# Kernel tuning notes

Hardware: AMD Instinct MI355X
Metric: run time of the kernel (lower is better)

The kernel has to match this reference:

```python
import jax, jax.numpy as jnp
import numpy as np

NUM_NODES = 200000   # graph size
E = 128              # embedding_size
B = 256              # batch of target nodes
M = 8                # num_metapaths
L = 64               # walk length (number of (n1,n2,e) triples per metapath)
NUM_EDGE_TYPE = 8
H = 8                # num_heads (hardcoded in module)


def setup_inputs() -> dict:
    key = jax.random.key(0)
    ks = jax.random.split(key, 10)
    # walks: last dim = (n1, n2, edge_type)
    n12 = jax.random.randint(ks[0], (B, M, L, 2), 0, NUM_NODES)
    ety = jax.random.randint(ks[1], (B, M, L, 1), 0, NUM_EDGE_TYPE)
    node_mp_walks = jnp.concatenate([n12, ety], axis=-1)
    node_idx = jax.random.randint(ks[2], (B,), 0, NUM_NODES)
    mp_type_idx = jnp.arange(M)
    # fc1(onehot(n)) == node_table[n] + fc1_b  (node_table = fc1.weight.T)
    node_table = jax.random.normal(ks[3], (NUM_NODES, E), dtype=jnp.float32) * 0.1
    fc1_b = jnp.zeros((E,), dtype=jnp.float32)
    edge_table = jax.random.normal(ks[4], (NUM_EDGE_TYPE, E), dtype=jnp.float32) * 0.1
    # Indexed_LinearFC_List: one (E,E) linear per metapath
    W_mp = jax.random.normal(ks[5], (M, E, E), dtype=jnp.float32) * 0.05
    b_mp = jnp.zeros((M, E), dtype=jnp.float32)
    # MultiheadAttention params (embed_dim=E, num_heads=H, eval mode -> no dropout)
    Wqkv = jax.random.normal(ks[6], (3 * E, E), dtype=jnp.float32) * 0.05
    bqkv = jnp.zeros((3 * E,), dtype=jnp.float32)
    Wo = jax.random.normal(ks[7], (E, E), dtype=jnp.float32) * 0.05
    bo = jnp.zeros((E,), dtype=jnp.float32)
    return dict(node_idx=node_idx, mp_type_idx=mp_type_idx, node_mp_walks=node_mp_walks,
                node_table=node_table, fc1_b=fc1_b, edge_table=edge_table,
                W_mp=W_mp, b_mp=b_mp, Wqkv=Wqkv, bqkv=bqkv, Wo=Wo, bo=bo)


def reference(node_idx, mp_type_idx, node_mp_walks, node_table, fc1_b, edge_table,
              W_mp, b_mp, Wqkv, bqkv, Wo, bo):
    n1 = node_mp_walks[..., 0]          # [B,M,L]
    n2 = node_mp_walks[..., 1]
    e = node_mp_walks[..., 2]
    # gather node/edge embeddings (fc1 over one-hot == table row + bias)
    n1_vec = node_table[n1] + fc1_b     # [B,M,L,E]
    n2_vec = node_table[n2] + fc1_b     # [B,M,L,E]
    edge_vec = edge_table[e]            # [B,M,L,E]
    # elementwise fuse + mean over walk steps
    mp_agg_0 = jnp.mean(n1_vec * n2_vec * edge_vec, axis=2)        # [B,M,E]
    # per-metapath indexed linear
    Wsel = W_mp[mp_type_idx]            # [M,E,E]
    bsel = b_mp[mp_type_idx]            # [M,E]
    mp_agg_1 = jnp.einsum('bme,meo->bmo', mp_agg_0, Wsel) + bsel   # [B,M,E]
    # self-attention over metapaths (torch MHA, seq-first layout: [M,B,E])
    x = jnp.transpose(mp_agg_1, (1, 0, 2))                         # [M,B,E]
    qkv = x @ Wqkv.T + bqkv                                        # [M,B,3E]
    q, k, v = jnp.split(qkv, 3, axis=-1)
    hd = E // H
    q = q.reshape(M, B, H, hd)
    k = k.reshape(M, B, H, hd)
    v = v.reshape(M, B, H, hd)
    scores = jnp.einsum('mbhd,nbhd->bhmn', q, k) / jnp.sqrt(jnp.float32(hd))
    attn = jax.nn.softmax(scores, axis=-1)                         # [B,H,M,M]
    o = jnp.einsum('bhmn,nbhd->mbhd', attn, v).reshape(M, B, E)
    attn_output = o @ Wo.T + bo                                    # [M,B,E]
    return attn_output
```

## Files before the change

### kernel.cpp

```cpp
#include <hip/hip_runtime.h>

#define B 256
#define M 8
#define L 64
#define E 128
#define H 8
#define HD 16
#define NET 8
#define E3 384

__global__ __launch_bounds__(256) void k_transpose(
    const float* __restrict__ Wqkv, const float* __restrict__ Wo,
    float* __restrict__ WqkvT, float* __restrict__ WoT) {
  int idx = blockIdx.x * 256 + threadIdx.x;
  if (idx < E * E3) {
    int e = idx / E3;
    int o = idx - e * E3;
    WqkvT[idx] = Wqkv[o * E + e];
  } else {
    int j = idx - E * E3;
    int e = j >> 7, o = j & 127;
    WoT[j] = Wo[o * E + e];
  }
}

__global__ __launch_bounds__(256) void k_gather(
    const int* __restrict__ walks, const float* __restrict__ node_table,
    const float* __restrict__ fc1_b, const float* __restrict__ edge_table,
    float* __restrict__ agg0) {
  __shared__ int s_idx[L * 3];
  __shared__ float s_et[NET * E];
  __shared__ float4 s_red[256];

  int r = blockIdx.x;
  int t = threadIdx.x;
  int g = t >> 5, lane = t & 31;

  if (t < L * 3) s_idx[t] = walks[r * (L * 3) + t];
  for (int i = t; i < NET * E; i += 256) s_et[i] = edge_table[i];
  __syncthreads();

  const float4* nt4 = (const float4*)node_table;
  float4 fb = ((const float4*)fc1_b)[lane];
  float4 acc = make_float4(0.f, 0.f, 0.f, 0.f);

  #pragma unroll
  for (int i = 0; i < 8; ++i) {
    int l = (i << 3) + g;
    int n1 = s_idx[3 * l];
    int n2 = s_idx[3 * l + 1];
    int et = s_idx[3 * l + 2];
    float4 a = nt4[n1 * 32 + lane];
    float4 c = nt4[n2 * 32 + lane];
    float4 ev = ((const float4*)(s_et + et * E))[lane];
    acc.x += (a.x + fb.x) * (c.x + fb.x) * ev.x;
    acc.y += (a.y + fb.y) * (c.y + fb.y) * ev.y;
    acc.z += (a.z + fb.z) * (c.z + fb.z) * ev.z;
    acc.w += (a.w + fb.w) * (c.w + fb.w) * ev.w;
  }
  s_red[t] = acc;
  __syncthreads();
  if (t < 32) {
    float4 s = s_red[t];
    #pragma unroll
    for (int gg = 1; gg < 8; ++gg) {
      float4 v = s_red[gg * 32 + t];
      s.x += v.x; s.y += v.y; s.z += v.z; s.w += v.w;
    }
    const float inv = 1.0f / (float)L;
    s.x *= inv; s.y *= inv; s.z *= inv; s.w *= inv;
    ((float4*)agg0)[r * 32 + t] = s;
  }
}

__global__ __launch_bounds__(128) void k_mplinear(
    const float* __restrict__ agg0, const int* __restrict__ mp_type_idx,
    const float* __restrict__ W_mp, const float* __restrict__ b_mp,
    float* __restrict__ agg1) {
  __shared__ float xs[8][E];
  int t = threadIdx.x;
  int m = blockIdx.y;
  int b0 = blockIdx.x * 8;
  int mp = mp_type_idx[m];
  #pragma unroll
  for (int j = 0; j < 8; ++j)
    xs[j][t] = agg0[((b0 + j) * M + m) * E + t];
  __syncthreads();
  float acc[8] = {0, 0, 0, 0, 0, 0, 0, 0};
  const float* W = W_mp + mp * E * E;
  for (int e = 0; e < E; ++e) {
    float w = W[e * E + t];
    #pragma unroll
    for (int j = 0; j < 8; ++j) acc[j] += xs[j][e] * w;
  }
  float bias = b_mp[mp * E + t];
  #pragma unroll
  for (int j = 0; j < 8; ++j)
    agg1[((b0 + j) * M + m) * E + t] = acc[j] + bias;
}

__global__ __launch_bounds__(128) void k_qkv(
    const float* __restrict__ agg1, const float* __restrict__ WqkvT,
    const float* __restrict__ bqkv, float* __restrict__ qkv) {
  __shared__ float xs[8][E];
  int t = threadIdx.x;
  int r0 = blockIdx.x * 8;
  int o = blockIdx.y * E + t;
  #pragma unroll
  for (int j = 0; j < 8; ++j)
    xs[j][t] = agg1[(r0 + j) * E + t];
  __syncthreads();
  float acc[8] = {0, 0, 0, 0, 0, 0, 0, 0};
  for (int e = 0; e < E; ++e) {
    float w = WqkvT[e * E3 + o];
    #pragma unroll
    for (int j = 0; j < 8; ++j) acc[j] += xs[j][e] * w;
  }
  float bias = bqkv[o];
  #pragma unroll
  for (int j = 0; j < 8; ++j)
    qkv[(r0 + j) * E3 + o] = acc[j] + bias;
}

__global__ __launch_bounds__(256) void k_attn(
    const float* __restrict__ qkv, const float* __restrict__ WoT,
    const float* __restrict__ bo, float* __restrict__ out) {
  __shared__ float s_qkv[M][E3 + 1];
  __shared__ float s_sc[H][M][M];
  __shared__ float s_o[M][E];
  int b = blockIdx.x;
  int t = threadIdx.x;

  #pragma unroll
  for (int i = 0; i < 12; ++i) {
    int idx = i * 256 + t;
    int mt = idx / E3;
    int col = idx - mt * E3;
    s_qkv[mt][col] = qkv[(b * M + mt) * E3 + col];
  }
  __syncthreads();

  #pragma unroll
  for (int i = 0; i < 2; ++i) {
    int idx = i * 256 + t;
    int h = idx >> 6;
    int mq = (idx >> 3) & 7;
    int n = idx & 7;
    float s = 0.f;
    #pragma unroll
    for (int d = 0; d < HD; ++d)
      s += s_qkv[mq][h * HD + d] * s_qkv[n][E + h * HD + d];
    s_sc[h][mq][n] = s * 0.25f;
  }
  __syncthreads();

  if (t < 64) {
    int h = t >> 3, mq = t & 7;
    float mx = -1e30f;
    #pragma unroll
    for (int n = 0; n < 8; ++n) mx = fmaxf(mx, s_sc[h][mq][n]);
    float ex[8];
    float sum = 0.f;
    #pragma unroll
    for (int n = 0; n < 8; ++n) { ex[n] = __expf(s_sc[h][mq][n] - mx); sum += ex[n]; }
    float inv = 1.0f / sum;
    #pragma unroll
    for (int n = 0; n < 8; ++n) s_sc[h][mq][n] = ex[n] * inv;
  }
  __syncthreads();

  #pragma unroll
  for (int i = 0; i < 4; ++i) {
    int idx = i * 256 + t;
    int mq = idx >> 7;
    int col = idx & 127;
    int h = col >> 4;
    float s = 0.f;
    #pragma unroll
    for (int n = 0; n < 8; ++n)
      s += s_sc[h][mq][n] * s_qkv[n][2 * E + col];
    s_o[mq][col] = s;
  }
  __syncthreads();

  int o = t & 127;
  int mbase = t >> 7;
  float accp[4] = {0, 0, 0, 0};
  for (int e = 0; e < E; ++e) {
    float w = WoT[e * E + o];
    #pragma unroll
    for (int i = 0; i < 4; ++i)
      accp[i] += s_o[2 * i + mbase][e] * w;
  }
  float bias = bo[o];
  #pragma unroll
  for (int i = 0; i < 4; ++i) {
    int mq = 2 * i + mbase;
    out[(mq * B + b) * E + o] = accp[i] + bias;
  }
}

extern "C" void kernel_launch(void* const* d_in, const int* in_sizes, int n_in,
                              void* d_out, int out_size, void* d_ws, size_t ws_size,
                              hipStream_t stream) {
  const int*   mp_type_idx = (const int*)d_in[1];
  const int*   walks       = (const int*)d_in[2];
  const float* node_table  = (const float*)d_in[3];
  const float* fc1_b       = (const float*)d_in[4];
  const float* edge_table  = (const float*)d_in[5];
  const float* W_mp        = (const float*)d_in[6];
  const float* b_mp        = (const float*)d_in[7];
  const float* Wqkv        = (const float*)d_in[8];
  const float* bqkv        = (const float*)d_in[9];
  const float* Wo          = (const float*)d_in[10];
  const float* bo          = (const float*)d_in[11];
  float* out = (float*)d_out;

  char* ws = (char*)d_ws;
  float* agg0  = (float*)(ws);
  float* agg1  = (float*)(ws + (1 << 20));
  float* qkvb  = (float*)(ws + (2 << 20));
  float* WqkvT = (float*)(ws + (5 << 20));
  float* WoT   = (float*)(ws + (5 << 20) + (256 << 10));

  k_transpose<<<dim3(256), dim3(256), 0, stream>>>(Wqkv, Wo, WqkvT, WoT);
  k_gather<<<dim3(B * M), dim3(256), 0, stream>>>(walks, node_table, fc1_b, edge_table, agg0);
  k_mplinear<<<dim3(32, 8), dim3(128), 0, stream>>>(agg0, mp_type_idx, W_mp, b_mp, agg1);
  k_qkv<<<dim3(256, 3), dim3(128), 0, stream>>>(agg1, WqkvT, bqkv, qkvb);
  k_attn<<<dim3(B), dim3(256), 0, stream>>>(qkvb, WoT, bo, out);
}
```

Measured before the change: 211.2 us.

## Fuse per-metapath linear and QKV projection into one kernel

```diff
diff --git a/kernel.cpp b/kernel.cpp
--- a/kernel.cpp
+++ b/kernel.cpp
@@ -73,53 +73,56 @@
   }
 }
 
-__global__ __launch_bounds__(128) void k_mplinear(
+__global__ __launch_bounds__(256) void k_mlp(
     const float* __restrict__ agg0, const int* __restrict__ mp_type_idx,
     const float* __restrict__ W_mp, const float* __restrict__ b_mp,
-    float* __restrict__ agg1) {
+    const float* __restrict__ WqkvT, const float* __restrict__ bqkv,
+    float* __restrict__ qkv) {
   __shared__ float xs[8][E];
+  __shared__ float ys[8][E];
   int t = threadIdx.x;
   int m = blockIdx.y;
   int b0 = blockIdx.x * 8;
   int mp = mp_type_idx[m];
-  #pragma unroll
-  for (int j = 0; j < 8; ++j)
-    xs[j][t] = agg0[((b0 + j) * M + m) * E + t];
-  __syncthreads();
-  float acc[8] = {0, 0, 0, 0, 0, 0, 0, 0};
-  const float* W = W_mp + mp * E * E;
-  for (int e = 0; e < E; ++e) {
-    float w = W[e * E + t];
-    #pragma unroll
-    for (int j = 0; j < 8; ++j) acc[j] += xs[j][e] * w;
-  }
-  float bias = b_mp[mp * E + t];
-  #pragma unroll
-  for (int j = 0; j < 8; ++j)
-    agg1[((b0 + j) * M + m) * E + t] = acc[j] + bias;
-}
-
-__global__ __launch_bounds__(128) void k_qkv(
-    const float* __restrict__ agg1, const float* __restrict__ WqkvT,
-    const float* __restrict__ bqkv, float* __restrict__ qkv) {
-  __shared__ float xs[8][E];
-  int t = threadIdx.x;
-  int r0 = blockIdx.x * 8;
-  int o = blockIdx.y * E + t;
-  #pragma unroll
-  for (int j = 0; j < 8; ++j)
-    xs[j][t] = agg1[(r0 + j) * E + t];
-  __syncthreads();
-  float acc[8] = {0, 0, 0, 0, 0, 0, 0, 0};
-  for (int e = 0; e < E; ++e) {
-    float w = WqkvT[e * E3 + o];
-    #pragma unroll
-    for (int j = 0; j < 8; ++j) acc[j] += xs[j][e] * w;
-  }
-  float bias = bqkv[o];
-  #pragma unroll
-  for (int j = 0; j < 8; ++j)
-    qkv[(r0 + j) * E3 + o] = acc[j] + bias;
+  int o = t & 127;
+  int half = t >> 7;
+
+  #pragma unroll
+  for (int i = 0; i < 4; ++i) {
+    int idx = i * 256 + t;
+    int j = idx >> 7, e = idx & 127;
+    xs[j][e] = agg0[((b0 + j) * M + m) * E + e];
+  }
+  __syncthreads();
+
+  {
+    const float* W = W_mp + mp * E * E;
+    float acc[4] = {0, 0, 0, 0};
+    for (int e = 0; e < E; ++e) {
+      float w = W[e * E + o];
+      #pragma unroll
+      for (int j = 0; j < 4; ++j) acc[j] += xs[half * 4 + j][e] * w;
+    }
+    float bias = b_mp[mp * E + o];
+    #pragma unroll
+    for (int j = 0; j < 4; ++j) ys[half * 4 + j][o] = acc[j] + bias;
+  }
+  __syncthreads();
+
+  #pragma unroll
+  for (int c = 0; c < 3; ++c) {
+    int oc = c * E + o;
+    float acc[4] = {0, 0, 0, 0};
+    for (int e = 0; e < E; ++e) {
+      float w = WqkvT[e * E3 + oc];
+      #pragma unroll
+      for (int j = 0; j < 4; ++j) acc[j] += ys[half * 4 + j][e] * w;
+    }
+    float bias = bqkv[oc];
+    #pragma unroll
+    for (int j = 0; j < 4; ++j)
+      qkv[((b0 + half * 4 + j) * M + m) * E3 + oc] = acc[j] + bias;
+  }
 }
 
 __global__ __launch_bounds__(256) void k_attn(
@@ -218,14 +221,12 @@
 
   char* ws = (char*)d_ws;
   float* agg0  = (float*)(ws);
-  float* agg1  = (float*)(ws + (1 << 20));
-  float* qkvb  = (float*)(ws + (2 << 20));
-  float* WqkvT = (float*)(ws + (5 << 20));
-  float* WoT   = (float*)(ws + (5 << 20) + (256 << 10));
+  float* qkvb  = (float*)(ws + (1 << 20));
+  float* WqkvT = (float*)(ws + (4 << 20));
+  float* WoT   = (float*)(ws + (4 << 20) + (256 << 10));
 
   k_transpose<<<dim3(256), dim3(256), 0, stream>>>(Wqkv, Wo, WqkvT, WoT);
   k_gather<<<dim3(B * M), dim3(256), 0, stream>>>(walks, node_table, fc1_b, edge_table, agg0);
-  k_mplinear<<<dim3(32, 8), dim3(128), 0, stream>>>(agg0, mp_type_idx, W_mp, b_mp, agg1);
-  k_qkv<<<dim3(256, 3), dim3(128), 0, stream>>>(agg1, WqkvT, bqkv, qkvb);
+  k_mlp<<<dim3(32, 8), dim3(256), 0, stream>>>(agg0, mp_type_idx, W_mp, b_mp, WqkvT, bqkv, qkvb);
   k_attn<<<dim3(B), dim3(256), 0, stream>>>(qkvb, WoT, bo, out);
 }
```

New measurement: 208.2 us. Within noise of the previous version (-1.4%).
